# Kernel tuning notes

Measured on AMD Instinct MI355X. Metric: run time of the kernel, lower is better.

Reference implementation:

```python
import jax, jax.numpy as jnp
import numpy as np

AFWD = 0.999
EPS = 1e-05


def setup_inputs() -> dict:
    key = jax.random.key(0)
    N, L = 8192, 4096
    x = jax.random.normal(key, (N, L), dtype=jnp.float32)
    m = jnp.zeros((L,), dtype=jnp.float32)    # EMA mean buffer (init 0)
    var = jnp.ones((L,), dtype=jnp.float32)   # EMA var buffer (init 1)
    return {"x": x, "m": m, "var": var}


def reference(x, m, var):
    """Online-normalization forward: sequential scan over the N (row) dim,
    vectorized over the L feature dim. Matches ControlNormalization.forward."""
    afwd = AFWD

    def step(carry, xt):
        mu, v = carry                      # each [L]
        scale = jnp.sqrt(v + EPS)
        d = xt - mu
        out = d / scale
        v_new = afwd * v + afwd * (1.0 - afwd) * d * d
        mu_new = mu + (1.0 - afwd) * d
        return (mu_new, v_new), out

    _, out = jax.lax.scan(step, (m, var), x)  # out: [N, L]
    return out
```

## Files before the change

kernel.cpp:

```cpp
#include <hip/hip_runtime.h>
#include <math.h>

#define AFWD 0.999f
#define ONE_MINUS_A (1.0f - 0.999f)
#define KCOEF (0.999f * (1.0f - 0.999f))
#define EPSV 1e-5f

typedef float floatx4 __attribute__((ext_vector_type(4)));

__global__ __launch_bounds__(256) void
passA(const float* __restrict__ x, float* __restrict__ Bmu,
      float* __restrict__ See, float* __restrict__ Te, int L4, int CH) {
  int idx  = blockIdx.x * blockDim.x + threadIdx.x;
  int col4 = idx % L4;
  int c    = idx / L4;
  const floatx4* xv = (const floatx4*)x;
  int base = c * CH * L4 + col4;

  float mu[4] = {0.f, 0.f, 0.f, 0.f};
  float s[4]  = {0.f, 0.f, 0.f, 0.f};
  float t[4]  = {0.f, 0.f, 0.f, 0.f};

#pragma unroll 4
  for (int i = 0; i < CH; ++i) {
    floatx4 v = xv[base + i * L4];
#pragma unroll
    for (int k = 0; k < 4; ++k) {
      float e = v[k] - mu[k];
      s[k] = fmaf(AFWD, s[k], e * e);
      t[k] += e;
      mu[k] = fmaf(ONE_MINUS_A, e, mu[k]);
    }
  }

  int o = c * L4 + col4;
  floatx4 om = {mu[0], mu[1], mu[2], mu[3]};
  floatx4 os = {s[0], s[1], s[2], s[3]};
  floatx4 ot = {t[0], t[1], t[2], t[3]};
  ((floatx4*)Bmu)[o] = om;
  ((floatx4*)See)[o] = os;
  ((floatx4*)Te)[o]  = ot;
}

__global__ __launch_bounds__(256) void
passB1(const float* __restrict__ Bmu, const float* __restrict__ See,
       const float* __restrict__ Te, float* __restrict__ Bsup,
       float* __restrict__ Ssup, float* __restrict__ Tsup, int L, int SUB,
       float A, float c_eg, float Sgg, float G) {
  int idx = blockIdx.x * blockDim.x + threadIdx.x;
  int l   = idx % L;
  int g   = idx / L;
  int base = g * SUB * L + l;

  float B = 0.f, T = 0.f, S = 0.f;
#pragma unroll 16
  for (int k = 0; k < SUB; ++k) {
    int o = base + k * L;
    float b2 = Bmu[o];
    float s2 = See[o];
    float t2 = Te[o];
    S = fmaf(A, S, fmaf(Sgg * B, B, fmaf(-2.0f * c_eg * B, t2, s2)));
    T = fmaf(-G, B, T + t2);
    B = fmaf(A, B, b2);
  }
  int o = g * L + l;
  Bsup[o] = B;
  Ssup[o] = S;
  Tsup[o] = T;
}

__global__ __launch_bounds__(256) void
passB2(const float* __restrict__ m, const float* __restrict__ var,
       const float* __restrict__ Bsup, const float* __restrict__ Ssup,
       const float* __restrict__ Tsup, float* __restrict__ Mg,
       float* __restrict__ Vg, int L, int GS, float Asup, float c_sup,
       float Sggsup) {
  int l = blockIdx.x * blockDim.x + threadIdx.x;
  float M = m[l];
  float V = var[l];
#pragma unroll 16
  for (int g = 0; g < GS; ++g) {
    int o = g * L + l;
    Mg[o] = M;
    Vg[o] = V;
    float b = Bsup[o];
    float s = Ssup[o];
    float t = Tsup[o];
    float sum = fmaf(M * M, Sggsup, fmaf(-2.0f * c_sup * M, t, s));
    V = fmaf(Asup, V, KCOEF * sum);
    M = fmaf(Asup, M, b);
  }
}

__global__ __launch_bounds__(256) void
passB3(const float* __restrict__ Bmu, const float* __restrict__ See,
       const float* __restrict__ Te, const float* __restrict__ Mg,
       const float* __restrict__ Vg, float* __restrict__ Ms,
       float* __restrict__ Vs, int L, int SUB, float A, float c_eg,
       float Sgg) {
  int idx = blockIdx.x * blockDim.x + threadIdx.x;
  int l   = idx % L;
  int g   = idx / L;
  int base = g * SUB * L + l;

  float M = Mg[g * L + l];
  float V = Vg[g * L + l];
#pragma unroll 16
  for (int k = 0; k < SUB; ++k) {
    int o = base + k * L;
    Ms[o] = M;
    Vs[o] = V;
    float b = Bmu[o];
    float s = See[o];
    float t = Te[o];
    float sum = fmaf(M * M, Sgg, fmaf(-2.0f * c_eg * M, t, s));
    V = fmaf(A, V, KCOEF * sum);
    M = fmaf(A, M, b);
  }
}

__global__ __launch_bounds__(256) void
passC(const float* __restrict__ x, const float* __restrict__ Ms,
      const float* __restrict__ Vs, float* __restrict__ out, int L4, int CH) {
  int idx  = blockIdx.x * blockDim.x + threadIdx.x;
  int col4 = idx % L4;
  int c    = idx / L4;
  const floatx4* xv = (const floatx4*)x;
  floatx4* ov = (floatx4*)out;
  int base = c * CH * L4 + col4;

  int o = c * L4 + col4;
  floatx4 m4 = ((const floatx4*)Ms)[o];
  floatx4 v4 = ((const floatx4*)Vs)[o];
  float mu[4] = {m4[0], m4[1], m4[2], m4[3]};
  float vv[4] = {v4[0], v4[1], v4[2], v4[3]};

#pragma unroll 4
  for (int i = 0; i < CH; ++i) {
    floatx4 v = xv[base + i * L4];
    floatx4 oe;
#pragma unroll
    for (int k = 0; k < 4; ++k) {
      float d = v[k] - mu[k];
      oe[k] = d * rsqrtf(vv[k] + EPSV);
      vv[k] = fmaf(AFWD, vv[k], KCOEF * (d * d));
      mu[k] = fmaf(ONE_MINUS_A, d, mu[k]);
    }
    __builtin_nontemporal_store(oe, &ov[base + i * L4]);
  }
}

extern "C" void kernel_launch(void* const* d_in, const int* in_sizes, int n_in,
                              void* d_out, int out_size, void* d_ws, size_t ws_size,
                              hipStream_t stream) {
  const float* x   = (const float*)d_in[0];
  const float* m   = (const float*)d_in[1];
  const float* var = (const float*)d_in[2];
  float* out = (float*)d_out;

  int L  = in_sizes[1];
  int N  = in_sizes[0] / L;
  int L4 = L / 4;

  int C = 256;
  while (C > 1 &&
         ((size_t)(5 * C + 5 * (C / 16 + 1)) * L * sizeof(float) > ws_size ||
          (N % C) != 0))
    C >>= 1;
  int CH = N / C;
  int SUB = (C >= 16) ? 16 : C;
  int GS  = C / SUB;

  double a = 0.999;
  float A    = (float)pow(a, (double)CH);
  float c_eg = (float)pow(a, (double)(CH - 1));
  float Sgg  = (float)(pow(a, (double)(CH - 1)) * (1.0 - pow(a, (double)CH)) / (1.0 - a));
  float G    = (float)((1.0 - pow(a, (double)CH)) / (1.0 - a));
  double nS = (double)SUB * CH;
  float Asup   = (float)pow(a, nS);
  float c_sup  = (float)pow(a, nS - 1.0);
  float Sggsup = (float)(pow(a, nS - 1.0) * (1.0 - pow(a, nS)) / (1.0 - a));

  float* ws  = (float*)d_ws;
  size_t CL  = (size_t)C * L;
  size_t GL  = (size_t)GS * L;
  float* Bmu  = ws;
  float* See  = ws + CL;
  float* Te   = ws + 2 * CL;
  float* Ms   = ws + 3 * CL;
  float* Vs   = ws + 4 * CL;
  float* Bsup = ws + 5 * CL;
  float* Ssup = Bsup + GL;
  float* Tsup = Bsup + 2 * GL;
  float* Mg   = Bsup + 3 * GL;
  float* Vg   = Bsup + 4 * GL;

  int threadsBig = C * L4;
  passA<<<threadsBig / 256, 256, 0, stream>>>(x, Bmu, See, Te, L4, CH);
  passB1<<<(L * GS) / 256, 256, 0, stream>>>(Bmu, See, Te, Bsup, Ssup, Tsup,
                                             L, SUB, A, c_eg, Sgg, G);
  passB2<<<L / 256, 256, 0, stream>>>(m, var, Bsup, Ssup, Tsup, Mg, Vg, L, GS,
                                      Asup, c_sup, Sggsup);
  passB3<<<(L * GS) / 256, 256, 0, stream>>>(Bmu, See, Te, Mg, Vg, Ms, Vs,
                                             L, SUB, A, c_eg, Sgg);
  passC<<<threadsBig / 256, 256, 0, stream>>>(x, Ms, Vs, out, L4, CH);
}
```

Baseline: 84.42 us.

## Fuse five scan passes into one cooperative kernel with grid syncs

```diff
diff --git a/kernel.cpp b/kernel.cpp
--- a/kernel.cpp
+++ b/kernel.cpp
@@ -1,5 +1,8 @@
 #include <hip/hip_runtime.h>
+#include <hip/hip_cooperative_groups.h>
 #include <math.h>
+
+namespace cg = cooperative_groups;
 
 #define AFWD 0.999f
 #define ONE_MINUS_A (1.0f - 0.999f)
@@ -7,6 +10,185 @@
 #define EPSV 1e-5f
 
 typedef float floatx4 __attribute__((ext_vector_type(4)));
+
+__global__ __launch_bounds__(256) void
+fused_cn3(const float* __restrict__ x, const float* __restrict__ m,
+          const float* __restrict__ var, float* __restrict__ out,
+          float* __restrict__ Bmu, float* __restrict__ See,
+          float* __restrict__ Te, float* __restrict__ Ms,
+          float* __restrict__ Vs, float* __restrict__ Bsup,
+          float* __restrict__ Ssup, float* __restrict__ Tsup,
+          float* __restrict__ Mg, float* __restrict__ Vg,
+          int L, int L4, int C, int CH, int SUB, int GS,
+          float A, float c_eg, float Sgg, float G,
+          float Asup, float c_sup, float Sggsup) {
+  cg::grid_group grid = cg::this_grid();
+
+  int idx  = blockIdx.x * blockDim.x + threadIdx.x;
+  int col4 = idx % L4;
+  int c    = idx / L4;
+  const floatx4* xv = (const floatx4*)x;
+  int base = c * CH * L4 + col4;
+  int o    = c * L4 + col4;
+
+  {
+    float mu[4] = {0.f, 0.f, 0.f, 0.f};
+    float s[4]  = {0.f, 0.f, 0.f, 0.f};
+    float t[4]  = {0.f, 0.f, 0.f, 0.f};
+#pragma unroll 1
+    for (int i = 0; i < CH; i += 4) {
+      floatx4 v0 = xv[base + (i + 0) * L4];
+      floatx4 v1 = xv[base + (i + 1) * L4];
+      floatx4 v2 = xv[base + (i + 2) * L4];
+      floatx4 v3 = xv[base + (i + 3) * L4];
+#pragma unroll
+      for (int k = 0; k < 4; ++k) {
+        float e = v0[k] - mu[k];
+        s[k] = fmaf(AFWD, s[k], e * e); t[k] += e;
+        mu[k] = fmaf(ONE_MINUS_A, e, mu[k]);
+      }
+#pragma unroll
+      for (int k = 0; k < 4; ++k) {
+        float e = v1[k] - mu[k];
+        s[k] = fmaf(AFWD, s[k], e * e); t[k] += e;
+        mu[k] = fmaf(ONE_MINUS_A, e, mu[k]);
+      }
+#pragma unroll
+      for (int k = 0; k < 4; ++k) {
+        float e = v2[k] - mu[k];
+        s[k] = fmaf(AFWD, s[k], e * e); t[k] += e;
+        mu[k] = fmaf(ONE_MINUS_A, e, mu[k]);
+      }
+#pragma unroll
+      for (int k = 0; k < 4; ++k) {
+        float e = v3[k] - mu[k];
+        s[k] = fmaf(AFWD, s[k], e * e); t[k] += e;
+        mu[k] = fmaf(ONE_MINUS_A, e, mu[k]);
+      }
+    }
+    floatx4 om = {mu[0], mu[1], mu[2], mu[3]};
+    floatx4 os = {s[0], s[1], s[2], s[3]};
+    floatx4 ot = {t[0], t[1], t[2], t[3]};
+    ((floatx4*)Bmu)[o] = om;
+    ((floatx4*)See)[o] = os;
+    ((floatx4*)Te)[o]  = ot;
+  }
+
+  grid.sync();
+
+  if (idx < L * GS) {
+    int l = idx % L;
+    int g = idx / L;
+    int b1 = g * SUB * L + l;
+    float B = 0.f, T = 0.f, S = 0.f;
+#pragma unroll 4
+    for (int k = 0; k < SUB; ++k) {
+      int oo = b1 + k * L;
+      float b2 = Bmu[oo];
+      float s2 = See[oo];
+      float t2 = Te[oo];
+      S = fmaf(A, S, fmaf(Sgg * B, B, fmaf(-2.0f * c_eg * B, t2, s2)));
+      T = fmaf(-G, B, T + t2);
+      B = fmaf(A, B, b2);
+    }
+    int oo = g * L + l;
+    Bsup[oo] = B;
+    Ssup[oo] = S;
+    Tsup[oo] = T;
+  }
+
+  grid.sync();
+
+  if (idx < L) {
+    int l = idx;
+    float M = m[l];
+    float V = var[l];
+#pragma unroll 4
+    for (int g = 0; g < GS; ++g) {
+      int oo = g * L + l;
+      Mg[oo] = M;
+      Vg[oo] = V;
+      float b = Bsup[oo];
+      float s = Ssup[oo];
+      float t = Tsup[oo];
+      float sum = fmaf(M * M, Sggsup, fmaf(-2.0f * c_sup * M, t, s));
+      V = fmaf(Asup, V, KCOEF * sum);
+      M = fmaf(Asup, M, b);
+    }
+  }
+
+  grid.sync();
+
+  if (idx < L * GS) {
+    int l = idx % L;
+    int g = idx / L;
+    int b3 = g * SUB * L + l;
+    float M = Mg[g * L + l];
+    float V = Vg[g * L + l];
+#pragma unroll 4
+    for (int k = 0; k < SUB; ++k) {
+      int oo = b3 + k * L;
+      Ms[oo] = M;
+      Vs[oo] = V;
+      float b = Bmu[oo];
+      float s = See[oo];
+      float t = Te[oo];
+      float sum = fmaf(M * M, Sgg, fmaf(-2.0f * c_eg * M, t, s));
+      V = fmaf(A, V, KCOEF * sum);
+      M = fmaf(A, M, b);
+    }
+  }
+
+  grid.sync();
+
+  {
+    floatx4* ov = (floatx4*)out;
+    floatx4 m4 = ((const floatx4*)Ms)[o];
+    floatx4 v4 = ((const floatx4*)Vs)[o];
+    float mu[4] = {m4[0], m4[1], m4[2], m4[3]};
+    float vv[4] = {v4[0], v4[1], v4[2], v4[3]};
+#pragma unroll 1
+    for (int i = 0; i < CH; i += 4) {
+      floatx4 v0 = xv[base + (i + 0) * L4];
+      floatx4 v1 = xv[base + (i + 1) * L4];
+      floatx4 v2 = xv[base + (i + 2) * L4];
+      floatx4 v3 = xv[base + (i + 3) * L4];
+      floatx4 o0, o1, o2, o3;
+#pragma unroll
+      for (int k = 0; k < 4; ++k) {
+        float d = v0[k] - mu[k];
+        o0[k] = d * rsqrtf(vv[k] + EPSV);
+        vv[k] = fmaf(AFWD, vv[k], KCOEF * (d * d));
+        mu[k] = fmaf(ONE_MINUS_A, d, mu[k]);
+      }
+#pragma unroll
+      for (int k = 0; k < 4; ++k) {
+        float d = v1[k] - mu[k];
+        o1[k] = d * rsqrtf(vv[k] + EPSV);
+        vv[k] = fmaf(AFWD, vv[k], KCOEF * (d * d));
+        mu[k] = fmaf(ONE_MINUS_A, d, mu[k]);
+      }
+#pragma unroll
+      for (int k = 0; k < 4; ++k) {
+        float d = v2[k] - mu[k];
+        o2[k] = d * rsqrtf(vv[k] + EPSV);
+        vv[k] = fmaf(AFWD, vv[k], KCOEF * (d * d));
+        mu[k] = fmaf(ONE_MINUS_A, d, mu[k]);
+      }
+#pragma unroll
+      for (int k = 0; k < 4; ++k) {
+        float d = v3[k] - mu[k];
+        o3[k] = d * rsqrtf(vv[k] + EPSV);
+        vv[k] = fmaf(AFWD, vv[k], KCOEF * (d * d));
+        mu[k] = fmaf(ONE_MINUS_A, d, mu[k]);
+      }
+      __builtin_nontemporal_store(o0, &ov[base + (i + 0) * L4]);
+      __builtin_nontemporal_store(o1, &ov[base + (i + 1) * L4]);
+      __builtin_nontemporal_store(o2, &ov[base + (i + 2) * L4]);
+      __builtin_nontemporal_store(o3, &ov[base + (i + 3) * L4]);
+    }
+  }
+}
 
 __global__ __launch_bounds__(256) void
 passA(const float* __restrict__ x, float* __restrict__ Bmu,
@@ -20,7 +202,6 @@
   float mu[4] = {0.f, 0.f, 0.f, 0.f};
   float s[4]  = {0.f, 0.f, 0.f, 0.f};
   float t[4]  = {0.f, 0.f, 0.f, 0.f};
-
 #pragma unroll 4
   for (int i = 0; i < CH; ++i) {
     floatx4 v = xv[base + i * L4];
@@ -32,7 +213,6 @@
       mu[k] = fmaf(ONE_MINUS_A, e, mu[k]);
     }
   }
-
   int o = c * L4 + col4;
   floatx4 om = {mu[0], mu[1], mu[2], mu[3]};
   floatx4 os = {s[0], s[1], s[2], s[3]};
@@ -51,9 +231,8 @@
   int l   = idx % L;
   int g   = idx / L;
   int base = g * SUB * L + l;
-
   float B = 0.f, T = 0.f, S = 0.f;
-#pragma unroll 16
+#pragma unroll 4
   for (int k = 0; k < SUB; ++k) {
     int o = base + k * L;
     float b2 = Bmu[o];
@@ -78,7 +257,7 @@
   int l = blockIdx.x * blockDim.x + threadIdx.x;
   float M = m[l];
   float V = var[l];
-#pragma unroll 16
+#pragma unroll 4
   for (int g = 0; g < GS; ++g) {
     int o = g * L + l;
     Mg[o] = M;
@@ -102,10 +281,9 @@
   int l   = idx % L;
   int g   = idx / L;
   int base = g * SUB * L + l;
-
   float M = Mg[g * L + l];
   float V = Vg[g * L + l];
-#pragma unroll 16
+#pragma unroll 4
   for (int k = 0; k < SUB; ++k) {
     int o = base + k * L;
     Ms[o] = M;
@@ -134,7 +312,6 @@
   floatx4 v4 = ((const floatx4*)Vs)[o];
   float mu[4] = {m4[0], m4[1], m4[2], m4[3]};
   float vv[4] = {v4[0], v4[1], v4[2], v4[3]};
-
 #pragma unroll 4
   for (int i = 0; i < CH; ++i) {
     floatx4 v = xv[base + i * L4];
@@ -162,10 +339,10 @@
   int N  = in_sizes[0] / L;
   int L4 = L / 4;
 
-  int C = 256;
+  int C = 128;
   while (C > 1 &&
          ((size_t)(5 * C + 5 * (C / 16 + 1)) * L * sizeof(float) > ws_size ||
-          (N % C) != 0))
+          (N % C) != 0 || ((N / C) % 4) != 0))
     C >>= 1;
   int CH = N / C;
   int SUB = (C >= 16) ? 16 : C;
@@ -196,12 +373,35 @@
   float* Vg   = Bsup + 4 * GL;
 
   int threadsBig = C * L4;
-  passA<<<threadsBig / 256, 256, 0, stream>>>(x, Bmu, See, Te, L4, CH);
+  int gridBlocks = threadsBig / 256;
+
+  int dev = 0, numCU = 0, maxPerCU = 0;
+  hipGetDevice(&dev);
+  hipDeviceGetAttribute(&numCU, hipDeviceAttributeMultiprocessorCount, dev);
+  hipOccupancyMaxActiveBlocksPerMultiprocessor(&maxPerCU, fused_cn3, 256, 0);
+  bool coop_ok = (maxPerCU > 0 && numCU > 0 &&
+                  (long)maxPerCU * numCU >= gridBlocks);
+
+  if (coop_ok) {
+    dim3 grid(gridBlocks), block(256);
+    void* args[] = {(void*)&x,    (void*)&m,    (void*)&var,  (void*)&out,
+                    (void*)&Bmu,  (void*)&See,  (void*)&Te,   (void*)&Ms,
+                    (void*)&Vs,   (void*)&Bsup, (void*)&Ssup, (void*)&Tsup,
+                    (void*)&Mg,   (void*)&Vg,   (void*)&L,    (void*)&L4,
+                    (void*)&C,    (void*)&CH,   (void*)&SUB,  (void*)&GS,
+                    (void*)&A,    (void*)&c_eg, (void*)&Sgg,  (void*)&G,
+                    (void*)&Asup, (void*)&c_sup, (void*)&Sggsup};
+    hipError_t err = hipLaunchCooperativeKernel((const void*)fused_cn3, grid,
+                                                block, args, 0, stream);
+    if (err == hipSuccess) return;
+  }
+
+  passA<<<gridBlocks, 256, 0, stream>>>(x, Bmu, See, Te, L4, CH);
   passB1<<<(L * GS) / 256, 256, 0, stream>>>(Bmu, See, Te, Bsup, Ssup, Tsup,
                                              L, SUB, A, c_eg, Sgg, G);
   passB2<<<L / 256, 256, 0, stream>>>(m, var, Bsup, Ssup, Tsup, Mg, Vg, L, GS,
                                       Asup, c_sup, Sggsup);
   passB3<<<(L * GS) / 256, 256, 0, stream>>>(Bmu, See, Te, Mg, Vg, Ms, Vs,
                                              L, SUB, A, c_eg, Sgg);
-  passC<<<threadsBig / 256, 256, 0, stream>>>(x, Ms, Vs, out, L4, CH);
-}
+  passC<<<gridBlocks, 256, 0, stream>>>(x, Ms, Vs, out, L4, CH);
+}
```

Result: slower. 300.1 us (+255.5%).
